# Performance work log

Measured on AMD Instinct MI355X. Metric: run time of the kernel, lower is better.

Reference implementation:

```python
import jax, jax.numpy as jnp
import numpy as np

N = 4096      # num nodes
D = 256       # hidden_dim
H = 4         # num attention heads (separate single-head MHA modules)
E = 131072    # num edges
EPS = 1e-5


def setup_inputs() -> dict:
    key = jax.random.key(0)
    ks = jax.random.split(key, 12)
    s = 0.02
    x = jax.random.normal(ks[0], (N, D), dtype=jnp.float32)
    edge_index = jax.random.randint(ks[1], (2, E), 0, N, dtype=jnp.int64)
    # per-head in_proj split into q/k/v, stacked over heads [H, D, D]
    Wq = jax.random.normal(ks[2], (H, D, D), dtype=jnp.float32) * s
    Wk = jax.random.normal(ks[3], (H, D, D), dtype=jnp.float32) * s
    Wv = jax.random.normal(ks[4], (H, D, D), dtype=jnp.float32) * s
    bq = jnp.zeros((H, D), dtype=jnp.float32)
    bk = jnp.zeros((H, D), dtype=jnp.float32)
    bv = jnp.zeros((H, D), dtype=jnp.float32)
    Wo = jax.random.normal(ks[5], (H, D, D), dtype=jnp.float32) * s  # per-head MHA out_proj
    bo = jnp.zeros((H, D), dtype=jnp.float32)
    Wp = jax.random.normal(ks[6], (D, H * D), dtype=jnp.float32) * s  # output_projection
    bp = jnp.zeros((D,), dtype=jnp.float32)
    gamma = jnp.ones((D,), dtype=jnp.float32)
    beta = jnp.zeros((D,), dtype=jnp.float32)
    return dict(x=x, edge_index=edge_index, Wq=Wq, bq=bq, Wk=Wk, bk=bk,
                Wv=Wv, bv=bv, Wo=Wo, bo=bo, Wp=Wp, bp=bp, gamma=gamma, beta=beta)


def _build_mask(edge_index, n):
    row, col = edge_index[0], edge_index[1]
    mask = jnp.full((n, n), -jnp.inf, dtype=jnp.float32)
    mask = mask.at[row, col].set(0.0)
    mask = mask.at[col, row].set(0.0)
    mask = mask.at[jnp.arange(n), jnp.arange(n)].set(0.0)
    return mask


def reference(x, edge_index, Wq, bq, Wk, bk, Wv, bv, Wo, bo, Wp, bp, gamma, beta):
    mask = _build_mask(edge_index, x.shape[0])  # [N, N] additive, -inf on non-edges
    # per-head projections (torch Linear: x @ W.T + b); h = head axis
    q = jnp.einsum('nd,hed->hne', x, Wq) + bq[:, None, :]
    k = jnp.einsum('nd,hed->hne', x, Wk) + bk[:, None, :]
    v = jnp.einsum('nd,hed->hne', x, Wv) + bv[:, None, :]
    scores = jnp.einsum('hne,hme->hnm', q, k) / jnp.sqrt(jnp.float32(D)) + mask[None]
    attn = jax.nn.softmax(scores, axis=-1)                    # [H, N, N]
    o = jnp.einsum('hnm,hme->hne', attn, v)                   # [H, N, D]
    head_out = jnp.einsum('hne,hfe->hnf', o, Wo) + bo[:, None, :]  # per-head out_proj
    concatenated = jnp.transpose(head_out, (1, 0, 2)).reshape(x.shape[0], H * D)
    out = concatenated @ Wp.T + bp                             # [N, D]
    mu = jnp.mean(out, axis=-1, keepdims=True)
    var = jnp.mean(jnp.square(out - mu), axis=-1, keepdims=True)
    return (out - mu) / jnp.sqrt(var + EPS) * gamma + beta
```

## Files before the change

### kernel.cpp

```cpp
#include <hip/hip_runtime.h>
#include <hip/hip_bf16.h>

#define N_NODES 4096
#define DIM 256
#define NHEAD 4
#define NEDGE 131072
#define MWORDS 128
#define MAXDEG 192
#define GBK 64

typedef unsigned short ushort_t;
typedef __attribute__((ext_vector_type(8))) short short8;
typedef __attribute__((ext_vector_type(4))) float f32x4;

__device__ __forceinline__ ushort_t f2bf(float f) {
    unsigned u = __float_as_uint(f);
    unsigned r = u + 0x7FFFu + ((u >> 16) & 1u);
    return (ushort_t)(r >> 16);
}
__device__ __forceinline__ float bf2f(ushort_t u) {
    return __uint_as_float((unsigned)u << 16);
}

__global__ __launch_bounds__(256) void build_mask_kernel(const int* __restrict__ ei,
                                                         unsigned* __restrict__ mask) {
    const int t = blockIdx.x * blockDim.x + threadIdx.x;
    if (t < NEDGE) {
        const int r = ei[t] & (N_NODES - 1);
        const int c = ei[NEDGE + t] & (N_NODES - 1);
        atomicOr(&mask[r * MWORDS + (c >> 5)], 1u << (c & 31));
        atomicOr(&mask[c * MWORDS + (r >> 5)], 1u << (r & 31));
    } else if (t < NEDGE + N_NODES) {
        const int i = t - NEDGE;
        atomicOr(&mask[i * MWORDS + (i >> 5)], 1u << (i & 31));
    }
}

__global__ __launch_bounds__(256) void convert_all_kernel(
    const float* __restrict__ x,  const float* __restrict__ Wq,
    const float* __restrict__ Wk, const float* __restrict__ Wv,
    const float* __restrict__ Wo, const float* __restrict__ Wp,
    ushort_t* __restrict__ xb, ushort_t* __restrict__ wstack,
    ushort_t* __restrict__ wob, ushort_t* __restrict__ wpb) {
    const int e = (blockIdx.x * blockDim.x + threadIdx.x) << 2;
    const float* src; ushort_t* dst; int off;
    if (e < 1048576)      { src = x;  dst = xb;              off = e; }
    else if (e < 1310720) { src = Wq; dst = wstack;          off = e - 1048576; }
    else if (e < 1572864) { src = Wk; dst = wstack + 262144; off = e - 1310720; }
    else if (e < 1835008) { src = Wv; dst = wstack + 524288; off = e - 1572864; }
    else if (e < 2097152) { src = Wo; dst = wob;             off = e - 1835008; }
    else                  { src = Wp; dst = wpb;             off = e - 2097152; }
    const float4 v = *(const float4*)(src + off);
    ushort4 r;
    r.x = f2bf(v.x); r.y = f2bf(v.y); r.z = f2bf(v.z); r.w = f2bf(v.w);
    *(ushort4*)(dst + off) = r;
}

template <int MODE>
__global__ __launch_bounds__(256) void mfma_gemm_kernel(
    const ushort_t* __restrict__ Wb, const ushort_t* __restrict__ Xb,
    const float* __restrict__ b0, const float* __restrict__ b1,
    const float* __restrict__ b2,
    ushort_t* __restrict__ qb, ushort_t* __restrict__ kvh,
    void* __restrict__ outp, int K) {
    __shared__ ushort_t Wt[128][GBK + 8];
    __shared__ ushort_t Xt[128][GBK + 8];
    const int tid = threadIdx.x;
    const int lane = tid & 63;
    const int wid = tid >> 6;
    const int wr = wid >> 1, wc = wid & 1;
    const int zoff = (MODE == 1) ? blockIdx.z : 0;
    const ushort_t* Wp_ = Wb + (size_t)zoff * (256 * 256);
    const ushort_t* Xp_ = Xb + (size_t)zoff * ((size_t)N_NODES * 256);
    const int chB = blockIdx.x * 128;
    const int ndB = blockIdx.y * 128;

    f32x4 acc[4][4] = {};

    for (int kt = 0; kt < K; kt += GBK) {
        short8 wreg[4], xreg[4];
#pragma unroll
        for (int i = 0; i < 4; ++i) {
            const int flat = tid + (i << 8);
            const int r = flat >> 3, s = flat & 7;
            wreg[i] = *(const short8*)(Wp_ + (size_t)(chB + r) * K + kt + (s << 3));
            xreg[i] = *(const short8*)(Xp_ + (size_t)(ndB + r) * K + kt + (s << 3));
        }
        __syncthreads();
#pragma unroll
        for (int i = 0; i < 4; ++i) {
            const int flat = tid + (i << 8);
            const int r = flat >> 3, s = flat & 7;
            *(short8*)&Wt[r][s << 3] = wreg[i];
            *(short8*)&Xt[r][s << 3] = xreg[i];
        }
        __syncthreads();
#pragma unroll
        for (int kk = 0; kk < 2; ++kk) {
            short8 af[4], bf[4];
            const int ko = (kk << 5) + ((lane >> 4) << 3);
#pragma unroll
            for (int m = 0; m < 4; ++m)
                af[m] = *(const short8*)&Wt[wr * 64 + m * 16 + (lane & 15)][ko];
#pragma unroll
            for (int n = 0; n < 4; ++n)
                bf[n] = *(const short8*)&Xt[wc * 64 + n * 16 + (lane & 15)][ko];
#pragma unroll
            for (int m = 0; m < 4; ++m)
#pragma unroll
                for (int n = 0; n < 4; ++n)
                    acc[m][n] = __builtin_amdgcn_mfma_f32_16x16x32_bf16(
                        af[m], bf[n], acc[m][n], 0, 0, 0);
        }
    }

    const int lhi = lane >> 4;
    const int llo = lane & 15;
    int op = 0, h = 0;
    if (MODE == 0) { op = chB >> 10; h = (chB >> 8) & 3; }
#pragma unroll
    for (int m = 0; m < 4; ++m) {
        const int ch = chB + wr * 64 + m * 16 + (lhi << 2);
        float4 bia;
        if (MODE == 0) {
            const float* bb = (op == 0 ? b0 : op == 1 ? b1 : b2) + (h << 8);
            bia = *(const float4*)&bb[ch & 255];
        } else if (MODE == 1) {
            bia = *(const float4*)&b0[(zoff << 8) + ch];
        } else {
            bia = *(const float4*)&b0[ch];
        }
#pragma unroll
        for (int n = 0; n < 4; ++n) {
            const int node = ndB + wc * 64 + n * 16 + llo;
            const float v0 = acc[m][n][0] + bia.x;
            const float v1 = acc[m][n][1] + bia.y;
            const float v2 = acc[m][n][2] + bia.z;
            const float v3 = acc[m][n][3] + bia.w;
            if (MODE == 2) {
                float4 r; r.x = v0; r.y = v1; r.z = v2; r.w = v3;
                *(float4*)&((float*)outp)[((size_t)node << 8) + ch] = r;
            } else {
                ushort4 r;
                r.x = f2bf(v0); r.y = f2bf(v1); r.z = f2bf(v2); r.w = f2bf(v3);
                if (MODE == 1) {
                    *(ushort4*)&((ushort_t*)outp)[(size_t)node * 1024 + (zoff << 8) + ch] = r;
                } else {
                    const int c = ch & 255;
                    if (op == 0)
                        *(ushort4*)&qb[(((size_t)h * N_NODES + node) << 8) + c] = r;
                    else if (op == 1)
                        *(ushort4*)&kvh[(((size_t)h * N_NODES + node) << 9) + c] = r;
                    else
                        *(ushort4*)&kvh[(((size_t)h * N_NODES + node) << 9) + 256 + c] = r;
                }
            }
        }
    }
}

__global__ __launch_bounds__(256) void attn_sparse_kernel(const unsigned* __restrict__ mask,
                                                          const ushort_t* __restrict__ qb,
                                                          const ushort_t* __restrict__ kvh,
                                                          ushort_t* __restrict__ ob) {
    __shared__ int nbr[4][MAXDEG];
    const int tid = threadIdx.x;
    const int w = tid >> 6;
    const int lane = tid & 63;
    const int xcd = blockIdx.x & 7;
    const int h = xcd >> 1;
    const int node = ((xcd & 1) << 11) + ((blockIdx.x >> 3) << 2) + w;

    const unsigned m0 = mask[node * MWORDS + lane];
    const unsigned m1 = mask[node * MWORDS + 64 + lane];
    const int c = __popc(m0) + __popc(m1);
    int s = c;
#pragma unroll
    for (int d = 1; d < 64; d <<= 1) {
        const int t = __shfl_up(s, d);
        if (lane >= d) s += t;
    }
    const int deg0 = __shfl(s, 63);
    const int deg = deg0 < MAXDEG ? deg0 : MAXDEG;
    int pos = s - c;
    unsigned mm = m0;
    int bj = lane << 5;
    while (mm) {
        const int b = __ffs(mm) - 1; mm &= mm - 1;
        if (pos < MAXDEG) nbr[w][pos] = bj + b;
        ++pos;
    }
    mm = m1; bj = (lane + 64) << 5;
    while (mm) {
        const int b = __ffs(mm) - 1; mm &= mm - 1;
        if (pos < MAXDEG) nbr[w][pos] = bj + b;
        ++pos;
    }
    __syncthreads();

    const int sub = lane >> 4;
    const int sl = lane & 15;

    const ushort_t* qp = qb + (((size_t)h * N_NODES + node) << 8) + (sl << 4);
    const short8 q0 = *(const short8*)qp;
    const short8 q1 = *(const short8*)(qp + 8);
    float qf[16];
#pragma unroll
    for (int i = 0; i < 8; ++i) {
        qf[i] = bf2f((ushort_t)q0[i]);
        qf[8 + i] = bf2f((ushort_t)q1[i]);
    }
    float oa[16];
#pragma unroll
    for (int i = 0; i < 16; ++i) oa[i] = 0.f;
    float denom = 0.f;

    const ushort_t* kbase = kvh + (((size_t)h * N_NODES) << 9) + (sl << 4);
    const float SC = 0.0625f * 1.44269504f;

    for (int n0 = 0; n0 < deg; n0 += 4) {
        const int idx = n0 + sub;
        const bool valid = idx < deg;
        const int j = nbr[w][valid ? idx : 0];
        const ushort_t* kp = kbase + ((size_t)j << 9);
        const short8 k0 = *(const short8*)kp;
        const short8 k1 = *(const short8*)(kp + 8);
        const short8 v0 = *(const short8*)(kp + 256);
        const short8 v1 = *(const short8*)(kp + 264);
        float p = 0.f;
#pragma unroll
        for (int i = 0; i < 8; ++i)
            p += qf[i] * bf2f((ushort_t)k0[i]) + qf[8 + i] * bf2f((ushort_t)k1[i]);
        p += __shfl_xor(p, 1);
        p += __shfl_xor(p, 2);
        p += __shfl_xor(p, 4);
        p += __shfl_xor(p, 8);
        const float wt = valid ? __builtin_amdgcn_exp2f(p * SC) : 0.f;
        denom += wt;
#pragma unroll
        for (int i = 0; i < 8; ++i) {
            oa[i] += wt * bf2f((ushort_t)v0[i]);
            oa[8 + i] += wt * bf2f((ushort_t)v1[i]);
        }
    }
    denom += __shfl_xor(denom, 16);
    denom += __shfl_xor(denom, 32);
#pragma unroll
    for (int i = 0; i < 16; ++i) {
        oa[i] += __shfl_xor(oa[i], 16);
        oa[i] += __shfl_xor(oa[i], 32);
    }
    if (sub == 0) {
        const float inv = 1.0f / denom;
        short8 r0, r1;
#pragma unroll
        for (int i = 0; i < 8; ++i) {
            r0[i] = (short)f2bf(oa[i] * inv);
            r1[i] = (short)f2bf(oa[8 + i] * inv);
        }
        ushort_t* op_ = ob + (((size_t)h * N_NODES + node) << 8) + (sl << 4);
        *(short8*)op_ = r0;
        *(short8*)(op_ + 8) = r1;
    }
}

__global__ __launch_bounds__(256) void layernorm_kernel(const float* __restrict__ inp,
                                                        const float* __restrict__ gamma,
                                                        const float* __restrict__ beta,
                                                        float* __restrict__ out) {
    const int row = (blockIdx.x << 2) + (threadIdx.x >> 6);
    const int lane = threadIdx.x & 63;
    const float4 xv = *(const float4*)&inp[row * DIM + (lane << 2)];
    float s = xv.x + xv.y + xv.z + xv.w;
#pragma unroll
    for (int off = 32; off; off >>= 1) s += __shfl_xor(s, off);
    const float mu = s * (1.0f / DIM);
    const float dx = xv.x - mu, dy = xv.y - mu, dz = xv.z - mu, dw = xv.w - mu;
    float sq = dx * dx + dy * dy + dz * dz + dw * dw;
#pragma unroll
    for (int off = 32; off; off >>= 1) sq += __shfl_xor(sq, off);
    const float inv = 1.0f / sqrtf(sq * (1.0f / DIM) + 1e-5f);
    const float4 gv = *(const float4*)&gamma[lane << 2];
    const float4 bv = *(const float4*)&beta[lane << 2];
    float4 r;
    r.x = dx * inv * gv.x + bv.x;
    r.y = dy * inv * gv.y + bv.y;
    r.z = dz * inv * gv.z + bv.z;
    r.w = dw * inv * gv.w + bv.w;
    *(float4*)&out[row * DIM + (lane << 2)] = r;
}

extern "C" void kernel_launch(void* const* d_in, const int* in_sizes, int n_in,
                              void* d_out, int out_size, void* d_ws, size_t ws_size,
                              hipStream_t stream) {
    const float* x     = (const float*)d_in[0];
    const int*   ei    = (const int*)d_in[1];
    const float* Wq    = (const float*)d_in[2];
    const float* bq    = (const float*)d_in[3];
    const float* Wk    = (const float*)d_in[4];
    const float* bk    = (const float*)d_in[5];
    const float* Wv    = (const float*)d_in[6];
    const float* bv    = (const float*)d_in[7];
    const float* Wo    = (const float*)d_in[8];
    const float* bo    = (const float*)d_in[9];
    const float* Wp    = (const float*)d_in[10];
    const float* bp    = (const float*)d_in[11];
    const float* gamma = (const float*)d_in[12];
    const float* beta  = (const float*)d_in[13];
    float* outf = (float*)d_out;

    char* ws = (char*)d_ws;
    unsigned* mask    = (unsigned*)(ws);
    ushort_t* xb      = (ushort_t*)(ws + (size_t)( 2 << 20));
    ushort_t* qb      = (ushort_t*)(ws + (size_t)( 4 << 20));
    ushort_t* kvh     = (ushort_t*)(ws + (size_t)(12 << 20));
    ushort_t* ob      = (ushort_t*)(ws + (size_t)(28 << 20));
    ushort_t* concatb = (ushort_t*)(ws + (size_t)(36 << 20));
    float*    outp    = (float*)  (ws + (size_t)(44 << 20));
    ushort_t* wstack  = (ushort_t*)(ws + (size_t)(48 << 20));
    ushort_t* wob     = (ushort_t*)(ws + (size_t)(50 << 20));
    ushort_t* wpb     = (ushort_t*)(ws + (size_t)(51 << 20));

    hipMemsetAsync(mask, 0, N_NODES * MWORDS * sizeof(unsigned), stream);
    build_mask_kernel<<<(NEDGE + N_NODES + 255) / 256, 256, 0, stream>>>(ei, mask);

    convert_all_kernel<<<2304, 256, 0, stream>>>(x, Wq, Wk, Wv, Wo, Wp,
                                                 xb, wstack, wob, wpb);

    mfma_gemm_kernel<0><<<dim3(24, 32), 256, 0, stream>>>(
        wstack, xb, bq, bk, bv, qb, kvh, nullptr, 256);

    attn_sparse_kernel<<<N_NODES, 256, 0, stream>>>(mask, qb, kvh, ob);

    mfma_gemm_kernel<1><<<dim3(2, 32, NHEAD), 256, 0, stream>>>(
        wob, ob, bo, nullptr, nullptr, nullptr, nullptr, concatb, 256);

    mfma_gemm_kernel<2><<<dim3(2, 32), 256, 0, stream>>>(
        wpb, concatb, bp, nullptr, nullptr, nullptr, nullptr, outp, 1024);

    layernorm_kernel<<<N_NODES / 4, 256, 0, stream>>>(outp, gamma, beta, outf);
}
```

Before: 201.7 us.

## Fuse output projection with LayerNorm and merge mask build into conversion kernel

Replaces the final projection GEMM plus separate LayerNorm with one kernel where each block computes all 256 output features for 64 nodes and reduces mean/variance in shared memory before writing normalized output. Also merges the edge-mask build and bf16 conversion into a single launch. This removes two kernel launches and the fp32 intermediate round trip. The fused kernel uses single-pass variance (E[x^2]-mu^2), which is slightly less numerically robust, and holds more registers per thread.

```diff
diff --git a/kernel.cpp b/kernel.cpp
--- a/kernel.cpp
+++ b/kernel.cpp
@@ -8,6 +8,7 @@
 #define MWORDS 128
 #define MAXDEG 192
 #define GBK 64
+#define MASK_BLOCKS 528
 
 typedef unsigned short ushort_t;
 typedef __attribute__((ext_vector_type(8))) short short8;
@@ -22,27 +23,28 @@
     return __uint_as_float((unsigned)u << 16);
 }
 
-__global__ __launch_bounds__(256) void build_mask_kernel(const int* __restrict__ ei,
-                                                         unsigned* __restrict__ mask) {
-    const int t = blockIdx.x * blockDim.x + threadIdx.x;
-    if (t < NEDGE) {
-        const int r = ei[t] & (N_NODES - 1);
-        const int c = ei[NEDGE + t] & (N_NODES - 1);
-        atomicOr(&mask[r * MWORDS + (c >> 5)], 1u << (c & 31));
-        atomicOr(&mask[c * MWORDS + (r >> 5)], 1u << (r & 31));
-    } else if (t < NEDGE + N_NODES) {
-        const int i = t - NEDGE;
-        atomicOr(&mask[i * MWORDS + (i >> 5)], 1u << (i & 31));
-    }
-}
-
-__global__ __launch_bounds__(256) void convert_all_kernel(
+__global__ __launch_bounds__(256) void init_kernel(
+    const int* __restrict__ ei, unsigned* __restrict__ mask,
     const float* __restrict__ x,  const float* __restrict__ Wq,
     const float* __restrict__ Wk, const float* __restrict__ Wv,
     const float* __restrict__ Wo, const float* __restrict__ Wp,
     ushort_t* __restrict__ xb, ushort_t* __restrict__ wstack,
     ushort_t* __restrict__ wob, ushort_t* __restrict__ wpb) {
-    const int e = (blockIdx.x * blockDim.x + threadIdx.x) << 2;
+    const int bid = blockIdx.x;
+    if (bid < MASK_BLOCKS) {
+        const int t = bid * 256 + threadIdx.x;
+        if (t < NEDGE) {
+            const int r = ei[t] & (N_NODES - 1);
+            const int c = ei[NEDGE + t] & (N_NODES - 1);
+            atomicOr(&mask[r * MWORDS + (c >> 5)], 1u << (c & 31));
+            atomicOr(&mask[c * MWORDS + (r >> 5)], 1u << (r & 31));
+        } else if (t < NEDGE + N_NODES) {
+            const int i = t - NEDGE;
+            atomicOr(&mask[i * MWORDS + (i >> 5)], 1u << (i & 31));
+        }
+        return;
+    }
+    const int e = ((bid - MASK_BLOCKS) * 256 + threadIdx.x) << 2;
     const float* src; ushort_t* dst; int off;
     if (e < 1048576)      { src = x;  dst = xb;              off = e; }
     else if (e < 1310720) { src = Wq; dst = wstack;          off = e - 1048576; }
@@ -125,10 +127,8 @@
         if (MODE == 0) {
             const float* bb = (op == 0 ? b0 : op == 1 ? b1 : b2) + (h << 8);
             bia = *(const float4*)&bb[ch & 255];
-        } else if (MODE == 1) {
+        } else {
             bia = *(const float4*)&b0[(zoff << 8) + ch];
-        } else {
-            bia = *(const float4*)&b0[ch];
         }
 #pragma unroll
         for (int n = 0; n < 4; ++n) {
@@ -137,24 +137,148 @@
             const float v1 = acc[m][n][1] + bia.y;
             const float v2 = acc[m][n][2] + bia.z;
             const float v3 = acc[m][n][3] + bia.w;
-            if (MODE == 2) {
-                float4 r; r.x = v0; r.y = v1; r.z = v2; r.w = v3;
-                *(float4*)&((float*)outp)[((size_t)node << 8) + ch] = r;
+            ushort4 r;
+            r.x = f2bf(v0); r.y = f2bf(v1); r.z = f2bf(v2); r.w = f2bf(v3);
+            if (MODE == 1) {
+                *(ushort4*)&((ushort_t*)outp)[(size_t)node * 1024 + (zoff << 8) + ch] = r;
             } else {
-                ushort4 r;
-                r.x = f2bf(v0); r.y = f2bf(v1); r.z = f2bf(v2); r.w = f2bf(v3);
-                if (MODE == 1) {
-                    *(ushort4*)&((ushort_t*)outp)[(size_t)node * 1024 + (zoff << 8) + ch] = r;
-                } else {
-                    const int c = ch & 255;
-                    if (op == 0)
-                        *(ushort4*)&qb[(((size_t)h * N_NODES + node) << 8) + c] = r;
-                    else if (op == 1)
-                        *(ushort4*)&kvh[(((size_t)h * N_NODES + node) << 9) + c] = r;
-                    else
-                        *(ushort4*)&kvh[(((size_t)h * N_NODES + node) << 9) + 256 + c] = r;
-                }
+                const int c = ch & 255;
+                if (op == 0)
+                    *(ushort4*)&qb[(((size_t)h * N_NODES + node) << 8) + c] = r;
+                else if (op == 1)
+                    *(ushort4*)&kvh[(((size_t)h * N_NODES + node) << 9) + c] = r;
+                else
+                    *(ushort4*)&kvh[(((size_t)h * N_NODES + node) << 9) + 256 + c] = r;
             }
+        }
+    }
+}
+
+__global__ __launch_bounds__(256) void final_ln_kernel(
+    const ushort_t* __restrict__ Wb,
+    const ushort_t* __restrict__ Xb,
+    const float* __restrict__ bp,
+    const float* __restrict__ gamma, const float* __restrict__ beta,
+    float* __restrict__ out) {
+    __shared__ ushort_t Wt[256][GBK + 8];
+    __shared__ ushort_t Xt[64][GBK + 8];
+    __shared__ float redS[4][64];
+    __shared__ float redQ[4][64];
+    const int tid = threadIdx.x;
+    const int lane = tid & 63;
+    const int wid = tid >> 6;
+    const int ndB = blockIdx.x * 64;
+
+    f32x4 acc[4][4] = {};
+
+    for (int kt = 0; kt < 1024; kt += GBK) {
+        short8 wreg[8], xreg[2];
+#pragma unroll
+        for (int i = 0; i < 8; ++i) {
+            const int flat = tid + (i << 8);
+            const int r = flat >> 3, s = flat & 7;
+            wreg[i] = *(const short8*)(Wb + (size_t)r * 1024 + kt + (s << 3));
+        }
+#pragma unroll
+        for (int i = 0; i < 2; ++i) {
+            const int flat = tid + (i << 8);
+            const int r = flat >> 3, s = flat & 7;
+            xreg[i] = *(const short8*)(Xb + (size_t)(ndB + r) * 1024 + kt + (s << 3));
+        }
+        __syncthreads();
+#pragma unroll
+        for (int i = 0; i < 8; ++i) {
+            const int flat = tid + (i << 8);
+            const int r = flat >> 3, s = flat & 7;
+            *(short8*)&Wt[r][s << 3] = wreg[i];
+        }
+#pragma unroll
+        for (int i = 0; i < 2; ++i) {
+            const int flat = tid + (i << 8);
+            const int r = flat >> 3, s = flat & 7;
+            *(short8*)&Xt[r][s << 3] = xreg[i];
+        }
+        __syncthreads();
+#pragma unroll
+        for (int kk = 0; kk < 2; ++kk) {
+            short8 af[4], bf[4];
+            const int ko = (kk << 5) + ((lane >> 4) << 3);
+#pragma unroll
+            for (int m = 0; m < 4; ++m)
+                af[m] = *(const short8*)&Wt[wid * 64 + m * 16 + (lane & 15)][ko];
+#pragma unroll
+            for (int n = 0; n < 4; ++n)
+                bf[n] = *(const short8*)&Xt[n * 16 + (lane & 15)][ko];
+#pragma unroll
+            for (int m = 0; m < 4; ++m)
+#pragma unroll
+                for (int n = 0; n < 4; ++n)
+                    acc[m][n] = __builtin_amdgcn_mfma_f32_16x16x32_bf16(
+                        af[m], bf[n], acc[m][n], 0, 0, 0);
+        }
+    }
+
+    const int lhi = lane >> 4;
+    const int llo = lane & 15;
+    float vout[4][4][4];
+    float psum[4] = {0.f, 0.f, 0.f, 0.f};
+    float psq[4]  = {0.f, 0.f, 0.f, 0.f};
+#pragma unroll
+    for (int m = 0; m < 4; ++m) {
+        const int f0 = wid * 64 + m * 16 + (lhi << 2);
+        const float4 bia = *(const float4*)&bp[f0];
+#pragma unroll
+        for (int n = 0; n < 4; ++n) {
+            const float v0 = acc[m][n][0] + bia.x;
+            const float v1 = acc[m][n][1] + bia.y;
+            const float v2 = acc[m][n][2] + bia.z;
+            const float v3 = acc[m][n][3] + bia.w;
+            vout[m][n][0] = v0; vout[m][n][1] = v1;
+            vout[m][n][2] = v2; vout[m][n][3] = v3;
+            psum[n] += v0 + v1 + v2 + v3;
+            psq[n]  += v0 * v0 + v1 * v1 + v2 * v2 + v3 * v3;
+        }
+    }
+#pragma unroll
+    for (int n = 0; n < 4; ++n) {
+        psum[n] += __shfl_xor(psum[n], 16);
+        psum[n] += __shfl_xor(psum[n], 32);
+        psq[n]  += __shfl_xor(psq[n], 16);
+        psq[n]  += __shfl_xor(psq[n], 32);
+    }
+    if (lhi == 0) {
+#pragma unroll
+        for (int n = 0; n < 4; ++n) {
+            redS[wid][n * 16 + llo] = psum[n];
+            redQ[wid][n * 16 + llo] = psq[n];
+        }
+    }
+    __syncthreads();
+    float mean[4], inv[4];
+#pragma unroll
+    for (int n = 0; n < 4; ++n) {
+        const int nd = n * 16 + llo;
+        const float S = redS[0][nd] + redS[1][nd] + redS[2][nd] + redS[3][nd];
+        const float Q = redQ[0][nd] + redQ[1][nd] + redQ[2][nd] + redQ[3][nd];
+        const float mu = S * (1.0f / DIM);
+        const float var = Q * (1.0f / DIM) - mu * mu;
+        mean[n] = mu;
+        inv[n] = 1.0f / sqrtf(var + 1e-5f);
+    }
+#pragma unroll
+    for (int m = 0; m < 4; ++m) {
+        const int f0 = wid * 64 + m * 16 + (lhi << 2);
+        const float4 gv = *(const float4*)&gamma[f0];
+        const float4 bv = *(const float4*)&beta[f0];
+#pragma unroll
+        for (int n = 0; n < 4; ++n) {
+            const int node = ndB + n * 16 + llo;
+            float4 r;
+            r.x = (vout[m][n][0] - mean[n]) * inv[n] * gv.x + bv.x;
+            r.y = (vout[m][n][1] - mean[n]) * inv[n] * gv.y + bv.y;
+            r.z = (vout[m][n][2] - mean[n]) * inv[n] * gv.z + bv.z;
+            r.w = (vout[m][n][3] - mean[n]) * inv[n] * gv.w + bv.w;
+            *(float4*)&out[(size_t)node * DIM + f0] = r;
         }
     }
 }
@@ -262,32 +386,6 @@
         *(short8*)op_ = r0;
         *(short8*)(op_ + 8) = r1;
     }
-}
-
-__global__ __launch_bounds__(256) void layernorm_kernel(const float* __restrict__ inp,
-                                                        const float* __restrict__ gamma,
-                                                        const float* __restrict__ beta,
-                                                        float* __restrict__ out) {
-    const int row = (blockIdx.x << 2) + (threadIdx.x >> 6);
-    const int lane = threadIdx.x & 63;
-    const float4 xv = *(const float4*)&inp[row * DIM + (lane << 2)];
-    float s = xv.x + xv.y + xv.z + xv.w;
-#pragma unroll
-    for (int off = 32; off; off >>= 1) s += __shfl_xor(s, off);
-    const float mu = s * (1.0f / DIM);
-    const float dx = xv.x - mu, dy = xv.y - mu, dz = xv.z - mu, dw = xv.w - mu;
-    float sq = dx * dx + dy * dy + dz * dz + dw * dw;
-#pragma unroll
-    for (int off = 32; off; off >>= 1) sq += __shfl_xor(sq, off);
-    const float inv = 1.0f / sqrtf(sq * (1.0f / DIM) + 1e-5f);
-    const float4 gv = *(const float4*)&gamma[lane << 2];
-    const float4 bv = *(const float4*)&beta[lane << 2];
-    float4 r;
-    r.x = dx * inv * gv.x + bv.x;
-    r.y = dy * inv * gv.y + bv.y;
-    r.z = dz * inv * gv.z + bv.z;
-    r.w = dw * inv * gv.w + bv.w;
-    *(float4*)&out[row * DIM + (lane << 2)] = r;
 }
 
 extern "C" void kernel_launch(void* const* d_in, const int* in_sizes, int n_in,
@@ -316,16 +414,14 @@
     ushort_t* kvh     = (ushort_t*)(ws + (size_t)(12 << 20));
     ushort_t* ob      = (ushort_t*)(ws + (size_t)(28 << 20));
     ushort_t* concatb = (ushort_t*)(ws + (size_t)(36 << 20));
-    float*    outp    = (float*)  (ws + (size_t)(44 << 20));
     ushort_t* wstack  = (ushort_t*)(ws + (size_t)(48 << 20));
     ushort_t* wob     = (ushort_t*)(ws + (size_t)(50 << 20));
     ushort_t* wpb     = (ushort_t*)(ws + (size_t)(51 << 20));
 
     hipMemsetAsync(mask, 0, N_NODES * MWORDS * sizeof(unsigned), stream);
-    build_mask_kernel<<<(NEDGE + N_NODES + 255) / 256, 256, 0, stream>>>(ei, mask);
-
-    convert_all_kernel<<<2304, 256, 0, stream>>>(x, Wq, Wk, Wv, Wo, Wp,
-                                                 xb, wstack, wob, wpb);
+
+    init_kernel<<<MASK_BLOCKS + 2304, 256, 0, stream>>>(
+        ei, mask, x, Wq, Wk, Wv, Wo, Wp, xb, wstack, wob, wpb);
 
     mfma_gemm_kernel<0><<<dim3(24, 32), 256, 0, stream>>>(
         wstack, xb, bq, bk, bv, qb, kvh, nullptr, 256);
@@ -335,8 +431,5 @@
     mfma_gemm_kernel<1><<<dim3(2, 32, NHEAD), 256, 0, stream>>>(
         wob, ob, bo, nullptr, nullptr, nullptr, nullptr, concatb, 256);
 
-    mfma_gemm_kernel<2><<<dim3(2, 32), 256, 0, stream>>>(
-        wpb, concatb, bp, nullptr, nullptr, nullptr, nullptr, outp, 1024);
-
-    layernorm_kernel<<<N_NODES / 4, 256, 0, stream>>>(outp, gamma, beta, outf);
-}
+    final_ln_kernel<<<64, 256, 0, stream>>>(wpb, concatb, bp, gamma, beta, outf);
+}
```

New measurement: 203.9 us. About the same (+1.1%).
